# Kernel tuning notes

Measured on AMD Instinct MI355X. Metric: run time of the kernel, lower is better.

The kernel has to match this reference:

```python
import jax, jax.numpy as jnp
import numpy as np

TOP_K = 0.7  # fraction of highest-loss samples kept


def setup_inputs() -> dict:
    key = jax.random.key(0)
    k1, k2 = jax.random.split(key)
    N, C = 262144, 128
    inp = jax.random.normal(k1, (N, C), dtype=jnp.float32)
    tgt = jax.random.randint(k2, (N,), 0, C, dtype=jnp.int64)
    return {"input": inp, "target": tgt}


def reference(input, target):
    # log-softmax over classes, one stable pass
    logp = jax.nn.log_softmax(input, axis=-1)  # [N, C]
    # per-row NLL: -logp[i, target[i]]
    per_row = -jnp.take_along_axis(logp, target[:, None], axis=-1)[:, 0]  # [N]
    k = int(TOP_K * per_row.shape[0])
    top_vals, _ = jax.lax.top_k(per_row, k)  # k largest losses
    return jnp.mean(top_vals)
```

## Files before the change

### kernel.cpp

```cpp
#include <hip/hip_runtime.h>


#define NCLASS 128
#define NREP 8
#define TPB 256
#define LOSS_GRID 2048
#define REF_GRID 256

struct Scalars {
  unsigned sel1;
  unsigned cnt_above;
  int krem;
};

__device__ __forceinline__ unsigned suffix_incl_u(unsigned x, int lane) {
#pragma unroll
  for (int off = 1; off < 64; off <<= 1) {
    unsigned v = __shfl_down(x, off, 64);
    if (lane + off < 64) x += v;
  }
  return x;
}

__device__ __forceinline__ double xor_reduce_d(double x) {
#pragma unroll
  for (int off = 32; off > 0; off >>= 1) x += __shfl_xor(x, off, 64);
  return x;
}

__device__ __forceinline__ void scan_desc(const unsigned* __restrict__ hist,
                                          int nbins, int nrep, unsigned Ktar,
                                          int* bin_out, unsigned* above_out) {
  const int lane = threadIdx.x;
  const int bpt = nbins >> 6;
  unsigned csum = 0;
  for (int rr = 0; rr < nrep; ++rr) {
    const unsigned* hp = hist + (size_t)rr * nbins + lane * bpt;
    for (int i = 0; i < bpt; ++i) csum += hp[i];
  }
  unsigned suf = suffix_incl_u(csum, lane);
  unsigned long long mask = __ballot(suf >= Ktar);
  int c = 63 - __builtin_clzll(mask);
  unsigned aboveC = __shfl(suf - csum, c, 64);

  unsigned h = 0;
  if (lane < bpt)
    for (int rr = 0; rr < nrep; ++rr)
      h += hist[(size_t)rr * nbins + c * bpt + lane];
  unsigned suf2 = suffix_incl_u(h, lane);
  unsigned long long mask2 = __ballot((lane < bpt) && (aboveC + suf2 >= Ktar));
  int u = 63 - __builtin_clzll(mask2);
  unsigned above = aboveC + __shfl(suf2 - h, u, 64);
  *bin_out = c * bpt + u;
  *above_out = above;
}

__global__ __launch_bounds__(TPB) void loss_hist_kernel(
    const float* __restrict__ x, const int* __restrict__ tgt,
    float* __restrict__ losses, unsigned* __restrict__ hist1, int N) {
  __shared__ unsigned lh[4096];
  for (int i = threadIdx.x; i < 4096; i += TPB) lh[i] = 0;
  __syncthreads();

  const int lane = threadIdx.x & 63;
  const int j = lane & 7;
  const int r = lane >> 3;
  const int gw = blockIdx.x * (TPB / 64) + (threadIdx.x >> 6);
  const int W = LOSS_GRID * (TPB / 64);
  for (int base = gw; base * 8 < N; base += W) {
    const int row = base * 8 + r;
    const float4* rp = (const float4*)(x + (size_t)row * NCLASS);
    float4 a = rp[j];
    float4 b = rp[j + 8];
    float4 c = rp[j + 16];
    float4 d = rp[j + 24];
    float xt = 0.0f;
    if (j == 0) {
      int t = tgt[row];
      xt = x[(size_t)row * NCLASS + t];
    }

    float m = fmaxf(fmaxf(fmaxf(a.x, a.y), fmaxf(a.z, a.w)),
                    fmaxf(fmaxf(b.x, b.y), fmaxf(b.z, b.w)));
    m = fmaxf(m, fmaxf(fmaxf(c.x, c.y), fmaxf(c.z, c.w)));
    m = fmaxf(m, fmaxf(fmaxf(d.x, d.y), fmaxf(d.z, d.w)));
    m = fmaxf(m, __shfl_xor(m, 1, 64));
    m = fmaxf(m, __shfl_xor(m, 2, 64));
    m = fmaxf(m, __shfl_xor(m, 4, 64));

    float s = __expf(a.x - m) + __expf(a.y - m) + __expf(a.z - m) + __expf(a.w - m)
            + __expf(b.x - m) + __expf(b.y - m) + __expf(b.z - m) + __expf(b.w - m)
            + __expf(c.x - m) + __expf(c.y - m) + __expf(c.z - m) + __expf(c.w - m)
            + __expf(d.x - m) + __expf(d.y - m) + __expf(d.z - m) + __expf(d.w - m);
    s += __shfl_xor(s, 1, 64);
    s += __shfl_xor(s, 2, 64);
    s += __shfl_xor(s, 4, 64);

    if (j == 0) {
      float loss = fmaxf(__logf(s) + m - xt, 0.0f);
      losses[row] = loss;
      atomicAdd(&lh[__float_as_uint(loss) >> 20], 1u);
    }
  }
  __syncthreads();
  unsigned* h = hist1 + (size_t)(blockIdx.x & (NREP - 1)) * 4096;
  for (int i = threadIdx.x; i < 4096; i += TPB) {
    unsigned v = lh[i];
    if (v) atomicAdd(&h[i], v);
  }
}

__global__ void scan1_kernel(const unsigned* __restrict__ hist1,
                             Scalars* __restrict__ sc, int K) {
  int bin; unsigned above;
  scan_desc(hist1, 4096, NREP, (unsigned)K, &bin, &above);
  if (threadIdx.x == 0) {
    sc->sel1 = (unsigned)bin;
    sc->cnt_above = above;
    sc->krem = K - (int)above;
  }
}

__global__ __launch_bounds__(TPB) void refine_kernel(
    const float* __restrict__ losses, unsigned* __restrict__ hist2,
    float* __restrict__ hsum2, unsigned* __restrict__ fine,
    const Scalars* __restrict__ sc, double* __restrict__ partials, int N) {
  __shared__ unsigned lc[1024];
  __shared__ float lsum[1024];
  __shared__ double dsm[TPB / 64];
  for (int i = threadIdx.x; i < 1024; i += TPB) { lc[i] = 0; lsum[i] = 0.0f; }
  __syncthreads();

  const int lane = threadIdx.x & 63;
  const unsigned sel1 = sc->sel1;
  const float4* L4 = (const float4*)losses;
  const int n4 = N >> 2;
  double accS1 = 0.0;
  for (int idx = blockIdx.x * TPB + threadIdx.x; idx < n4;
       idx += REF_GRID * TPB) {
    float4 v = L4[idx];
#pragma unroll
    for (int comp = 0; comp < 4; ++comp) {
      float f = (comp == 0) ? v.x : (comp == 1) ? v.y : (comp == 2) ? v.z : v.w;
      unsigned b = __float_as_uint(f);
      unsigned hi = b >> 20;
      if (hi > sel1) {
        accS1 += (double)f;
      } else if (hi == sel1) {
        atomicAdd(&lc[(b >> 10) & 1023u], 1u);
        atomicAdd(&lsum[(b >> 10) & 1023u], f);
        atomicAdd(&fine[b & 0xFFFFFu], 1u);
      }
    }
  }
  accS1 = xor_reduce_d(accS1);
  if (lane == 0) dsm[threadIdx.x >> 6] = accS1;
  __syncthreads();
  if (threadIdx.x == 0)
    partials[blockIdx.x] = dsm[0] + dsm[1] + dsm[2] + dsm[3];

  unsigned* h = hist2 + (size_t)(blockIdx.x & (NREP - 1)) * 1024;
  for (int i = threadIdx.x; i < 1024; i += TPB) {
    unsigned c = lc[i];
    if (c) { atomicAdd(&h[i], c); atomicAdd(&hsum2[i], lsum[i]); }
  }
}

__global__ __launch_bounds__(TPB) void final_kernel(
    const unsigned* __restrict__ hist2, const float* __restrict__ hsum2,
    const unsigned* __restrict__ fine, const Scalars* __restrict__ sc,
    const double* __restrict__ partials, float* __restrict__ out, int K) {
  __shared__ double dsm[TPB / 64];
  __shared__ double S1sh;
  const int lane = threadIdx.x & 63;

  double s1 = partials[threadIdx.x];
  s1 = xor_reduce_d(s1);
  if (lane == 0) dsm[threadIdx.x >> 6] = s1;
  __syncthreads();
  if (threadIdx.x == 0) S1sh = dsm[0] + dsm[1] + dsm[2] + dsm[3];
  __syncthreads();

  if (threadIdx.x < 64) {
    const unsigned sel1 = sc->sel1;
    const unsigned krem = (unsigned)sc->krem;
    int sel2; unsigned above2;
    scan_desc(hist2, 1024, NREP, krem, &sel2, &above2);
    const unsigned krem2 = krem - above2;

    double s2 = 0.0;
    for (int b = sel2 + 1 + lane; b < 1024; b += 64) s2 += (double)hsum2[b];
    s2 = xor_reduce_d(s2);

    const unsigned* freg = fine + ((size_t)sel2 << 10);
    int bin3; unsigned above3;
    scan_desc(freg, 1024, 1, krem2, &bin3, &above3);

    const unsigned pfx = (sel1 << 20) | ((unsigned)sel2 << 10);
    double s3 = 0.0;
    for (int t = bin3 + 1 + lane; t < 1024; t += 64) {
      unsigned c = freg[t];
      if (c) s3 += (double)c * (double)__uint_as_float(pfx | (unsigned)t);
    }
    s3 = xor_reduce_d(s3);

    if (lane == 0) {
      unsigned thr_bits = pfx | (unsigned)bin3;
      unsigned cnt_gt = sc->cnt_above + above2 + above3;
      double thrv = (double)__uint_as_float(thr_bits);
      double mean = (S1sh + s2 + s3 +
                     (double)(K - (int)cnt_gt) * thrv) / (double)K;
      *out = (float)mean;
    }
  }
}

extern "C" void kernel_launch(void* const* d_in, const int* in_sizes, int n_in,
                              void* d_out, int out_size, void* d_ws, size_t ws_size,
                              hipStream_t stream) {
  const float* x = (const float*)d_in[0];
  const int* tgt = (const int*)d_in[1];
  float* out = (float*)d_out;
  int N = in_sizes[1];
  int K = (int)(0.7 * (double)N);

  char* ws = (char*)d_ws;
  const size_t OFF_H1 = (size_t)N * 4;
  const size_t OFF_H2 = OFF_H1 + (size_t)NREP * 4096 * 4;
  const size_t OFF_HS = OFF_H2 + (size_t)NREP * 1024 * 4;
  const size_t OFF_SC = OFF_HS + 1024 * 4;
  const size_t OFF_FN = OFF_SC + 128;
  const size_t OFF_PT = OFF_FN + (size_t)(1u << 20) * 4;

  float* losses = (float*)ws;
  unsigned* hist1 = (unsigned*)(ws + OFF_H1);
  unsigned* hist2 = (unsigned*)(ws + OFF_H2);
  float* hsum2 = (float*)(ws + OFF_HS);
  Scalars* sc = (Scalars*)(ws + OFF_SC);
  unsigned* fine = (unsigned*)(ws + OFF_FN);
  double* partials = (double*)(ws + OFF_PT);

  hipMemsetAsync(ws + OFF_H1, 0, OFF_PT - OFF_H1, stream);

  loss_hist_kernel<<<LOSS_GRID, TPB, 0, stream>>>(x, tgt, losses, hist1, N);
  scan1_kernel<<<1, 64, 0, stream>>>(hist1, sc, K);
  refine_kernel<<<REF_GRID, TPB, 0, stream>>>(losses, hist2, hsum2, fine, sc,
                                              partials, N);
  final_kernel<<<1, TPB, 0, stream>>>(hist2, hsum2, fine, sc, partials, out, K);
}
```

Baseline: 214.1 us.

## Map 16 rows per wave without grid-stride, fold scan1 into refine kernel

The loss kernel now assigns 4 lanes per row and 16 rows per wave, with each lane loading 8 float4s. It launches one block per 64 rows instead of a fixed grid-stride loop, which gives more loads in flight per thread. The separate single-wave scan1 kernel is removed: every refine block redundantly scans hist1 to find the coarse bin, and block 0 writes the scalars. This saves one launch and its dependency gap, at the cost of each of the 256 blocks rereading the 4096x8 histogram. The new mapping assumes N is a multiple of 64 and has no bounds check.

```diff
diff --git a/kernel.cpp b/kernel.cpp
--- a/kernel.cpp
+++ b/kernel.cpp
@@ -4,7 +4,6 @@
 #define NCLASS 128
 #define NREP 8
 #define TPB 256
-#define LOSS_GRID 2048
 #define REF_GRID 256
 
 struct Scalars {
@@ -63,44 +62,52 @@
   __syncthreads();
 
   const int lane = threadIdx.x & 63;
-  const int j = lane & 7;
-  const int r = lane >> 3;
-  const int gw = blockIdx.x * (TPB / 64) + (threadIdx.x >> 6);
-  const int W = LOSS_GRID * (TPB / 64);
-  for (int base = gw; base * 8 < N; base += W) {
-    const int row = base * 8 + r;
-    const float4* rp = (const float4*)(x + (size_t)row * NCLASS);
-    float4 a = rp[j];
-    float4 b = rp[j + 8];
-    float4 c = rp[j + 16];
-    float4 d = rp[j + 24];
-    float xt = 0.0f;
-    if (j == 0) {
-      int t = tgt[row];
-      xt = x[(size_t)row * NCLASS + t];
-    }
-
-    float m = fmaxf(fmaxf(fmaxf(a.x, a.y), fmaxf(a.z, a.w)),
-                    fmaxf(fmaxf(b.x, b.y), fmaxf(b.z, b.w)));
-    m = fmaxf(m, fmaxf(fmaxf(c.x, c.y), fmaxf(c.z, c.w)));
-    m = fmaxf(m, fmaxf(fmaxf(d.x, d.y), fmaxf(d.z, d.w)));
-    m = fmaxf(m, __shfl_xor(m, 1, 64));
-    m = fmaxf(m, __shfl_xor(m, 2, 64));
-    m = fmaxf(m, __shfl_xor(m, 4, 64));
-
-    float s = __expf(a.x - m) + __expf(a.y - m) + __expf(a.z - m) + __expf(a.w - m)
-            + __expf(b.x - m) + __expf(b.y - m) + __expf(b.z - m) + __expf(b.w - m)
-            + __expf(c.x - m) + __expf(c.y - m) + __expf(c.z - m) + __expf(c.w - m)
-            + __expf(d.x - m) + __expf(d.y - m) + __expf(d.z - m) + __expf(d.w - m);
-    s += __shfl_xor(s, 1, 64);
-    s += __shfl_xor(s, 2, 64);
-    s += __shfl_xor(s, 4, 64);
-
-    if (j == 0) {
-      float loss = fmaxf(__logf(s) + m - xt, 0.0f);
-      losses[row] = loss;
-      atomicAdd(&lh[__float_as_uint(loss) >> 20], 1u);
-    }
+  const int j = lane & 3;
+  const int r = lane >> 2;
+  const int wave = blockIdx.x * (TPB / 64) + (threadIdx.x >> 6);
+  const int row = wave * 16 + r;
+
+  const float4* rp = (const float4*)(x + (size_t)row * NCLASS);
+  float4 v0 = rp[j];
+  float4 v1 = rp[j + 4];
+  float4 v2 = rp[j + 8];
+  float4 v3 = rp[j + 12];
+  float4 v4 = rp[j + 16];
+  float4 v5 = rp[j + 20];
+  float4 v6 = rp[j + 24];
+  float4 v7 = rp[j + 28];
+  float xt = 0.0f;
+  if (j == 0) {
+    int t = tgt[row];
+    xt = x[(size_t)row * NCLASS + t];
+  }
+
+  float m = fmaxf(fmaxf(fmaxf(v0.x, v0.y), fmaxf(v0.z, v0.w)),
+                  fmaxf(fmaxf(v1.x, v1.y), fmaxf(v1.z, v1.w)));
+  m = fmaxf(m, fmaxf(fmaxf(fmaxf(v2.x, v2.y), fmaxf(v2.z, v2.w)),
+                     fmaxf(fmaxf(v3.x, v3.y), fmaxf(v3.z, v3.w))));
+  m = fmaxf(m, fmaxf(fmaxf(fmaxf(v4.x, v4.y), fmaxf(v4.z, v4.w)),
+                     fmaxf(fmaxf(v5.x, v5.y), fmaxf(v5.z, v5.w))));
+  m = fmaxf(m, fmaxf(fmaxf(fmaxf(v6.x, v6.y), fmaxf(v6.z, v6.w)),
+                     fmaxf(fmaxf(v7.x, v7.y), fmaxf(v7.z, v7.w))));
+  m = fmaxf(m, __shfl_xor(m, 1, 64));
+  m = fmaxf(m, __shfl_xor(m, 2, 64));
+
+  float s = __expf(v0.x - m) + __expf(v0.y - m) + __expf(v0.z - m) + __expf(v0.w - m)
+          + __expf(v1.x - m) + __expf(v1.y - m) + __expf(v1.z - m) + __expf(v1.w - m)
+          + __expf(v2.x - m) + __expf(v2.y - m) + __expf(v2.z - m) + __expf(v2.w - m)
+          + __expf(v3.x - m) + __expf(v3.y - m) + __expf(v3.z - m) + __expf(v3.w - m)
+          + __expf(v4.x - m) + __expf(v4.y - m) + __expf(v4.z - m) + __expf(v4.w - m)
+          + __expf(v5.x - m) + __expf(v5.y - m) + __expf(v5.z - m) + __expf(v5.w - m)
+          + __expf(v6.x - m) + __expf(v6.y - m) + __expf(v6.z - m) + __expf(v6.w - m)
+          + __expf(v7.x - m) + __expf(v7.y - m) + __expf(v7.z - m) + __expf(v7.w - m);
+  s += __shfl_xor(s, 1, 64);
+  s += __shfl_xor(s, 2, 64);
+
+  if (j == 0) {
+    float loss = fmaxf(__logf(s) + m - xt, 0.0f);
+    losses[row] = loss;
+    atomicAdd(&lh[__float_as_uint(loss) >> 20], 1u);
   }
   __syncthreads();
   unsigned* h = hist1 + (size_t)(blockIdx.x & (NREP - 1)) * 4096;
@@ -110,29 +117,33 @@
   }
 }
 
-__global__ void scan1_kernel(const unsigned* __restrict__ hist1,
-                             Scalars* __restrict__ sc, int K) {
-  int bin; unsigned above;
-  scan_desc(hist1, 4096, NREP, (unsigned)K, &bin, &above);
-  if (threadIdx.x == 0) {
-    sc->sel1 = (unsigned)bin;
-    sc->cnt_above = above;
-    sc->krem = K - (int)above;
-  }
-}
-
 __global__ __launch_bounds__(TPB) void refine_kernel(
-    const float* __restrict__ losses, unsigned* __restrict__ hist2,
-    float* __restrict__ hsum2, unsigned* __restrict__ fine,
-    const Scalars* __restrict__ sc, double* __restrict__ partials, int N) {
+    const float* __restrict__ losses, const unsigned* __restrict__ hist1,
+    unsigned* __restrict__ hist2, float* __restrict__ hsum2,
+    unsigned* __restrict__ fine, Scalars* __restrict__ sc,
+    double* __restrict__ partials, int N, int K) {
   __shared__ unsigned lc[1024];
   __shared__ float lsum[1024];
   __shared__ double dsm[TPB / 64];
+  __shared__ unsigned sel1_sh;
   for (int i = threadIdx.x; i < 1024; i += TPB) { lc[i] = 0; lsum[i] = 0.0f; }
+
+  if (threadIdx.x < 64) {
+    int bin; unsigned above;
+    scan_desc(hist1, 4096, NREP, (unsigned)K, &bin, &above);
+    if (threadIdx.x == 0) {
+      sel1_sh = (unsigned)bin;
+      if (blockIdx.x == 0) {
+        sc->sel1 = (unsigned)bin;
+        sc->cnt_above = above;
+        sc->krem = K - (int)above;
+      }
+    }
+  }
   __syncthreads();
 
   const int lane = threadIdx.x & 63;
-  const unsigned sel1 = sc->sel1;
+  const unsigned sel1 = sel1_sh;
   const float4* L4 = (const float4*)losses;
   const int n4 = N >> 2;
   double accS1 = 0.0;
@@ -242,9 +253,8 @@
 
   hipMemsetAsync(ws + OFF_H1, 0, OFF_PT - OFF_H1, stream);
 
-  loss_hist_kernel<<<LOSS_GRID, TPB, 0, stream>>>(x, tgt, losses, hist1, N);
-  scan1_kernel<<<1, 64, 0, stream>>>(hist1, sc, K);
-  refine_kernel<<<REF_GRID, TPB, 0, stream>>>(losses, hist2, hsum2, fine, sc,
-                                              partials, N);
+  loss_hist_kernel<<<N / 64, TPB, 0, stream>>>(x, tgt, losses, hist1, N);
+  refine_kernel<<<REF_GRID, TPB, 0, stream>>>(losses, hist1, hist2, hsum2,
+                                              fine, sc, partials, N, K);
   final_kernel<<<1, TPB, 0, stream>>>(hist2, hsum2, fine, sc, partials, out, K);
 }
```

Result: no change. 211.5 us (-1.2%).
